# Performance work log

Measured on AMD Instinct MI355X. Metric: run time of the kernel, lower is better.

Reference implementation:

```python
import jax, jax.numpy as jnp
import numpy as np

N, E = 20000, 320000          # nodes, edges
R, B = 9, 9                   # num_relations, num_bases
IN, HID, OUT = 128, 256, 64   # feature dims
EPS = 1e-5                    # LayerNorm eps


def layer_norm(h, gamma, beta):
    mu = jnp.mean(h, axis=-1, keepdims=True)
    var = jnp.var(h, axis=-1, keepdims=True)
    return (h - mu) * jax.lax.rsqrt(var + EPS) * gamma + beta


def rgcn_conv(x, src, dst, etype, bases, comp, root, bias, aggr):
    # basis decomposition: W_r = sum_b comp[r,b] * bases[b]
    W = jnp.einsum('rb,bio->rio', comp, bases)          # [R, in, out]
    xW = jnp.einsum('ni,rio->rno', x, W)                # [R, N, out]
    msg = xW[etype, src]                                # [E, out] gather per edge
    if aggr == 'max':
        agg = jax.ops.segment_max(msg, dst, num_segments=N)
        agg = jnp.where(jnp.isfinite(agg), agg, 0.0)    # empty segments -> 0
    else:
        agg = jax.ops.segment_sum(msg, dst, num_segments=N)
    return agg + x @ root + bias


def setup_inputs() -> dict:
    key = jax.random.key(0)
    ks = jax.random.split(key, 12)
    rn = lambda k, s, sc=0.05: jax.random.normal(k, s, jnp.float32) * sc
    return {
        'x': jax.random.normal(ks[0], (N, IN), jnp.float32),
        'edge_index': jax.random.randint(ks[1], (2, E), 0, N),
        'edge_type': jax.random.randint(ks[2], (E,), 0, R),
        # conv1 params
        'bases1': rn(ks[3], (B, IN, HID)),
        'comp1': rn(ks[4], (R, B), 0.3),
        'root1': rn(ks[5], (IN, HID)),
        'bias1': jnp.zeros((HID,), jnp.float32),
        'g1': jnp.ones((HID,), jnp.float32),
        'b1': jnp.zeros((HID,), jnp.float32),
        # conv2 params
        'bases2': rn(ks[6], (B, HID, OUT)),
        'comp2': rn(ks[7], (R, B), 0.3),
        'root2': rn(ks[8], (HID, OUT)),
        'bias2': jnp.zeros((OUT,), jnp.float32),
        'g2': jnp.ones((OUT,), jnp.float32),
        'b2': jnp.zeros((OUT,), jnp.float32),
    }


def reference(x, edge_index, edge_type, bases1, comp1, root1, bias1, g1, b1,
              bases2, comp2, root2, bias2, g2, b2):
    src, dst = edge_index[0], edge_index[1]
    h = rgcn_conv(x, src, dst, edge_type, bases1, comp1, root1, bias1, 'max')
    h = jax.nn.relu(layer_norm(h, g1, b1))
    # eval mode: edge dropout and feature dropout are identity
    h = rgcn_conv(h, src, dst, edge_type, bases2, comp2, root2, bias2, 'add')
    h = layer_norm(h, g2, b2)
    return jax.nn.log_softmax(h, axis=1)
```

## Files before the change

kernel.cpp:

```cpp
#include <hip/hip_runtime.h>
#include <math.h>

#define NN 20000
#define NE 320000
#define NREL 9
#define NBASES 9
#define D_IN 128
#define D_HID 256
#define D_OUT 64
#define LN_EPS 1e-5f

#define N1 (NREL * D_HID + D_HID)
#define N2 (NREL * D_OUT + D_OUT)
#define NBLK ((NN + 255) / 256)

typedef __attribute__((ext_vector_type(8))) short bf16x8;
typedef __attribute__((ext_vector_type(4))) float f32x4;

__device__ inline ushort f2b(float f) {
    unsigned u = __float_as_uint(f);
    return (ushort)((u + 0x7FFFu + ((u >> 16) & 1u)) >> 16);
}
__device__ inline float b2f(ushort h) { return __uint_as_float(((unsigned)h) << 16); }
__device__ inline unsigned pack2bf(float f0, float f1) {
    return (unsigned)f2b(f0) | ((unsigned)f2b(f1) << 16);
}

__global__ __launch_bounds__(256) void prep_all(
    const float* __restrict__ bases1, const float* __restrict__ comp1, const float* __restrict__ root1,
    const float* __restrict__ bases2, const float* __restrict__ comp2, const float* __restrict__ root2,
    const float* __restrict__ x,
    ushort* __restrict__ w1t, ushort* __restrict__ w2t, ushort* __restrict__ xbf)
{
    const int SZ1 = N1 * D_IN;
    const int SZ2 = N2 * D_HID;
    const int SZX = NN * D_IN;
    int tid = blockIdx.x * 256 + threadIdx.x;
    if (tid < SZ1) {
        int n = tid >> 7, k = tid & 127;
        float s;
        if (n < NREL * D_HID) {
            int r = n >> 8, o = n & 255;
            s = 0.f;
            #pragma unroll
            for (int b = 0; b < NBASES; b++)
                s += comp1[r * NBASES + b] * bases1[(b * D_IN + k) * D_HID + o];
        } else {
            s = root1[k * D_HID + (n - NREL * D_HID)];
        }
        w1t[tid] = f2b(s);
    } else if (tid < SZ1 + SZ2) {
        int j = tid - SZ1;
        int n = j >> 8, k = j & 255;
        float s;
        if (n < NREL * D_OUT) {
            int r = n >> 6, o = n & 63;
            s = 0.f;
            #pragma unroll
            for (int b = 0; b < NBASES; b++)
                s += comp2[r * NBASES + b] * bases2[(b * D_HID + k) * D_OUT + o];
        } else {
            s = root2[k * D_OUT + (n - NREL * D_OUT)];
        }
        w2t[j] = f2b(s);
    } else if (tid < SZ1 + SZ2 + SZX) {
        int j = tid - SZ1 - SZ2;
        xbf[j] = f2b(x[j]);
    }
}

__global__ __launch_bounds__(256) void hist_dst(const int* __restrict__ dst, int* __restrict__ deg)
{
    int e = blockIdx.x * 256 + threadIdx.x;
    if (e < NE) atomicAdd(&deg[dst[e]], 1);
}

__global__ __launch_bounds__(256) void scan_blk(
    const int* __restrict__ deg, int* __restrict__ local, int* __restrict__ bsum)
{
    __shared__ int wsum[4];
    int tid = threadIdx.x, lane = tid & 63, w = tid >> 6;
    int i = blockIdx.x * 256 + tid;
    int v = (i < NN) ? deg[i] : 0;
    int x = v;
    #pragma unroll
    for (int d = 1; d < 64; d <<= 1) {
        int y = __shfl_up(x, d, 64);
        if (lane >= d) x += y;
    }
    if (lane == 63) wsum[w] = x;
    __syncthreads();
    int woff = 0;
    for (int j = 0; j < w; j++) woff += wsum[j];
    if (i < NN) local[i] = woff + x - v;
    if (tid == 255) bsum[blockIdx.x] = woff + x;
}

__global__ __launch_bounds__(64) void scan_top(const int* __restrict__ bsum, int* __restrict__ boff)
{
    int lane = threadIdx.x;
    int carry = 0;
    for (int base = 0; base < NBLK; base += 64) {
        int i = base + lane;
        int v = (i < NBLK) ? bsum[i] : 0;
        int x = v;
        #pragma unroll
        for (int d = 1; d < 64; d <<= 1) {
            int y = __shfl_up(x, d, 64);
            if (lane >= d) x += y;
        }
        if (i < NBLK) boff[i] = carry + x - v;
        carry += __shfl(x, 63, 64);
    }
}

__global__ __launch_bounds__(256) void scan_fin(
    const int* __restrict__ local, const int* __restrict__ boff,
    int* __restrict__ offs, int* __restrict__ cursor)
{
    int i = blockIdx.x * 256 + threadIdx.x;
    if (i < NN) {
        int o = local[i] + boff[i >> 8];
        offs[i] = o;
        cursor[i] = o;
    }
    if (i == NN) offs[NN] = NE;
}

__global__ __launch_bounds__(256) void scatter_ep(
    const int* __restrict__ src, const int* __restrict__ dst, const int* __restrict__ etype,
    int* __restrict__ cursor, int* __restrict__ ep1, int* __restrict__ ep2)
{
    int e = blockIdx.x * 256 + threadIdx.x;
    if (e >= NE) return;
    int d = dst[e];
    int s = src[e], r = etype[e];
    int pos = atomicAdd(&cursor[d], 1);
    ep1[pos] = s * N1 + r * D_HID;
    ep2[pos] = s * N2 + r * D_OUT;
}

__global__ __launch_bounds__(256) void gemm_bf16(
    const ushort* __restrict__ A, const ushort* __restrict__ Bt, ushort* __restrict__ C,
    int M, int N, int K)
{
    __shared__ ushort As[512 * 8];
    __shared__ ushort Bs[512 * 8];

    int tid = threadIdx.x;
    int lane = tid & 63, w = tid >> 6;
    int wm = w >> 1, wn = w & 1;
    int row0 = blockIdx.y * 128, col0 = blockIdx.x * 128;

    int mr = lane & 15, kc = lane >> 4;
    const ushort* ga[2];
    const ushort* gb[2];
    #pragma unroll
    for (int j = 0; j < 2; j++) {
        int g = w * 2 + j;
        int row = min(row0 + g * 16 + mr, M - 1);
        ga[j] = &A[(size_t)row * K + kc * 8];
        int col = col0 + g * 16 + mr;
        gb[j] = &Bt[(size_t)col * K + kc * 8];
    }

    f32x4 acc[4][4];
    #pragma unroll
    for (int mt = 0; mt < 4; mt++)
        #pragma unroll
        for (int nt = 0; nt < 4; nt++)
            acc[mt][nt] = (f32x4){0.f, 0.f, 0.f, 0.f};

    for (int k0 = 0; k0 < K; k0 += 32) {
        #pragma unroll
        for (int j = 0; j < 2; j++) {
            int sbase = (w * 2 + j) * 64;
            __builtin_amdgcn_global_load_lds(
                (const __attribute__((address_space(1))) unsigned int*)ga[j],
                (__attribute__((address_space(3))) unsigned int*)&As[(size_t)sbase * 8],
                16, 0, 0);
            __builtin_amdgcn_global_load_lds(
                (const __attribute__((address_space(1))) unsigned int*)gb[j],
                (__attribute__((address_space(3))) unsigned int*)&Bs[(size_t)sbase * 8],
                16, 0, 0);
            ga[j] += 32;
            gb[j] += 32;
        }
        __syncthreads();

        bf16x8 af[4], bfr[4];
        #pragma unroll
        for (int mt = 0; mt < 4; mt++)
            af[mt] = *(const bf16x8*)&As[(size_t)(((wm * 4 + mt) * 64) + lane) * 8];
        #pragma unroll
        for (int nt = 0; nt < 4; nt++)
            bfr[nt] = *(const bf16x8*)&Bs[(size_t)(((wn * 4 + nt) * 64) + lane) * 8];
        #pragma unroll
        for (int mt = 0; mt < 4; mt++)
            #pragma unroll
            for (int nt = 0; nt < 4; nt++)
                acc[mt][nt] = __builtin_amdgcn_mfma_f32_16x16x32_bf16(
                    bfr[nt], af[mt], acc[mt][nt], 0, 0, 0);
        __syncthreads();
    }

    int q = lane >> 4, cm = lane & 15;
    #pragma unroll
    for (int mt = 0; mt < 4; mt++) {
        int gr = row0 + wm * 64 + mt * 16 + cm;
        if (gr < M) {
            #pragma unroll
            for (int nt = 0; nt < 4; nt++) {
                int gc = col0 + wn * 64 + nt * 16 + q * 4;
                uint2 o;
                o.x = pack2bf(acc[mt][nt][0], acc[mt][nt][1]);
                o.y = pack2bf(acc[mt][nt][2], acc[mt][nt][3]);
                *(uint2*)&C[(size_t)gr * N + gc] = o;
            }
        }
    }
}

__global__ __launch_bounds__(256) void gather1(
    const ushort* __restrict__ xw1, const int* __restrict__ offs, const int* __restrict__ ep1,
    const float* __restrict__ bias, const float* __restrict__ g, const float* __restrict__ b,
    ushort* __restrict__ h)
{
    int n = blockIdx.x * 4 + (threadIdx.x >> 6);
    if (n >= NN) return;
    int lane = threadIdx.x & 63;
    int lane4 = lane * 4;
    int e0 = __builtin_amdgcn_readfirstlane(offs[n]);
    int e1 = __builtin_amdgcn_readfirstlane(offs[n + 1]);

    float m0 = -INFINITY, m1 = -INFINITY, m2 = -INFINITY, m3 = -INFINITY;
    int e = e0;
    for (; e + 8 <= e1; e += 8) {
        int p[8];
        #pragma unroll
        for (int j = 0; j < 8; j++) p[j] = ep1[e + j];
        ushort4 v[8];
        #pragma unroll
        for (int j = 0; j < 8; j++) v[j] = *(const ushort4*)&xw1[(size_t)(p[j] + lane4)];
        #pragma unroll
        for (int j = 0; j < 8; j++) {
            m0 = fmaxf(m0, b2f(v[j].x)); m1 = fmaxf(m1, b2f(v[j].y));
            m2 = fmaxf(m2, b2f(v[j].z)); m3 = fmaxf(m3, b2f(v[j].w));
        }
    }
    for (; e + 2 <= e1; e += 2) {
        int pa = ep1[e], pb = ep1[e + 1];
        ushort4 va = *(const ushort4*)&xw1[(size_t)(pa + lane4)];
        ushort4 vb = *(const ushort4*)&xw1[(size_t)(pb + lane4)];
        m0 = fmaxf(m0, fmaxf(b2f(va.x), b2f(vb.x)));
        m1 = fmaxf(m1, fmaxf(b2f(va.y), b2f(vb.y)));
        m2 = fmaxf(m2, fmaxf(b2f(va.z), b2f(vb.z)));
        m3 = fmaxf(m3, fmaxf(b2f(va.w), b2f(vb.w)));
    }
    for (; e < e1; e++) {
        int p = ep1[e];
        ushort4 v = *(const ushort4*)&xw1[(size_t)(p + lane4)];
        m0 = fmaxf(m0, b2f(v.x)); m1 = fmaxf(m1, b2f(v.y));
        m2 = fmaxf(m2, b2f(v.z)); m3 = fmaxf(m3, b2f(v.w));
    }
    if (e1 == e0) { m0 = m1 = m2 = m3 = 0.f; }

    ushort4 rt = *(const ushort4*)&xw1[(size_t)n * N1 + NREL * D_HID + lane4];
    int c = lane4;
    float t0 = m0 + b2f(rt.x) + bias[c + 0];
    float t1 = m1 + b2f(rt.y) + bias[c + 1];
    float t2 = m2 + b2f(rt.z) + bias[c + 2];
    float t3 = m3 + b2f(rt.w) + bias[c + 3];

    float s = t0 + t1 + t2 + t3;
    float s2 = t0 * t0 + t1 * t1 + t2 * t2 + t3 * t3;
    #pragma unroll
    for (int m = 32; m >= 1; m >>= 1) {
        s  += __shfl_xor(s,  m, 64);
        s2 += __shfl_xor(s2, m, 64);
    }
    float mu = s * (1.f / D_HID);
    float var = s2 * (1.f / D_HID) - mu * mu;
    float rs = rsqrtf(var + LN_EPS);

    ushort4 o;
    o.x = f2b(fmaxf((t0 - mu) * rs * g[c + 0] + b[c + 0], 0.f));
    o.y = f2b(fmaxf((t1 - mu) * rs * g[c + 1] + b[c + 1], 0.f));
    o.z = f2b(fmaxf((t2 - mu) * rs * g[c + 2] + b[c + 2], 0.f));
    o.w = f2b(fmaxf((t3 - mu) * rs * g[c + 3] + b[c + 3], 0.f));
    *(ushort4*)&h[(size_t)n * D_HID + c] = o;
}

__global__ __launch_bounds__(256) void gather2(
    const ushort* __restrict__ xw2, const int* __restrict__ offs, const int* __restrict__ ep2,
    const float* __restrict__ bias, const float* __restrict__ g, const float* __restrict__ b,
    float* __restrict__ out)
{
    int n = blockIdx.x * 4 + (threadIdx.x >> 6);
    if (n >= NN) return;
    int lane = threadIdx.x & 63;
    int e0 = __builtin_amdgcn_readfirstlane(offs[n]);
    int e1 = __builtin_amdgcn_readfirstlane(offs[n + 1]);

    float s = 0.f;
    int e = e0;
    for (; e + 4 <= e1; e += 4) {
        int p0 = ep2[e + 0], p1 = ep2[e + 1], p2 = ep2[e + 2], p3 = ep2[e + 3];
        float a0 = b2f(xw2[(size_t)(p0 + lane)]);
        float a1 = b2f(xw2[(size_t)(p1 + lane)]);
        float a2 = b2f(xw2[(size_t)(p2 + lane)]);
        float a3 = b2f(xw2[(size_t)(p3 + lane)]);
        s += (a0 + a1) + (a2 + a3);
    }
    for (; e < e1; e++) {
        s += b2f(xw2[(size_t)(ep2[e] + lane)]);
    }
    float v = s + b2f(xw2[(size_t)n * N2 + NREL * D_OUT + lane]) + bias[lane];

    float sm = v, s2 = v * v;
    #pragma unroll
    for (int m = 32; m >= 1; m >>= 1) {
        sm += __shfl_xor(sm, m, 64);
        s2 += __shfl_xor(s2, m, 64);
    }
    float mu = sm * (1.f / D_OUT);
    float var = s2 * (1.f / D_OUT) - mu * mu;
    float y = (v - mu) * rsqrtf(var + LN_EPS) * g[lane] + b[lane];

    float mx = y;
    #pragma unroll
    for (int m = 32; m >= 1; m >>= 1) mx = fmaxf(mx, __shfl_xor(mx, m, 64));
    float ex = __expf(y - mx);
    float se = ex;
    #pragma unroll
    for (int m = 32; m >= 1; m >>= 1) se += __shfl_xor(se, m, 64);
    out[(size_t)n * D_OUT + lane] = y - mx - logf(se);
}

extern "C" void kernel_launch(void* const* d_in, const int* in_sizes, int n_in,
                              void* d_out, int out_size, void* d_ws, size_t ws_size,
                              hipStream_t stream)
{
    const float* x      = (const float*)d_in[0];
    const int*   eidx   = (const int*)  d_in[1];
    const int*   etype  = (const int*)  d_in[2];
    const float* bases1 = (const float*)d_in[3];
    const float* comp1  = (const float*)d_in[4];
    const float* root1  = (const float*)d_in[5];
    const float* bias1  = (const float*)d_in[6];
    const float* g1     = (const float*)d_in[7];
    const float* b1     = (const float*)d_in[8];
    const float* bases2 = (const float*)d_in[9];
    const float* comp2  = (const float*)d_in[10];
    const float* root2  = (const float*)d_in[11];
    const float* bias2  = (const float*)d_in[12];
    const float* g2     = (const float*)d_in[13];
    const float* b2     = (const float*)d_in[14];

    const int* src = eidx;
    const int* dst = eidx + NE;

    char* p = (char*)d_ws;
    auto alloc = [&](size_t bytes) -> char* {
        char* r = p;
        p += (bytes + 255) & ~(size_t)255;
        return r;
    };
    ushort* xbf    = (ushort*)alloc((size_t)NN * D_IN * 2);
    ushort* w1t    = (ushort*)alloc((size_t)N1 * D_IN * 2);
    ushort* w2t    = (ushort*)alloc((size_t)N2 * D_HID * 2);
    ushort* xw1    = (ushort*)alloc((size_t)NN * N1 * 2);
    ushort* xw2    = (ushort*)alloc((size_t)NN * N2 * 2);
    ushort* h      = (ushort*)alloc((size_t)NN * D_HID * 2);
    int*    deg    = (int*)   alloc((size_t)NN * 4);
    int*    local  = (int*)   alloc((size_t)NN * 4);
    int*    bsum   = (int*)   alloc((size_t)NBLK * 4);
    int*    boff   = (int*)   alloc((size_t)NBLK * 4);
    int*    offs   = (int*)   alloc((size_t)(NN + 1) * 4);
    int*    cursor = (int*)   alloc((size_t)NN * 4);
    int*    ep1    = (int*)   alloc((size_t)NE * 4);
    int*    ep2    = (int*)   alloc((size_t)NE * 4);

    const int SZP = N1 * D_IN + N2 * D_HID + NN * D_IN;
    prep_all<<<(SZP + 255) / 256, 256, 0, stream>>>(
        bases1, comp1, root1, bases2, comp2, root2, x, w1t, w2t, xbf);

    hipMemsetAsync(deg, 0, (size_t)NN * 4, stream);
    hist_dst<<<(NE + 255) / 256, 256, 0, stream>>>(dst, deg);
    scan_blk<<<NBLK, 256, 0, stream>>>(deg, local, bsum);
    scan_top<<<1, 64, 0, stream>>>(bsum, boff);
    scan_fin<<<NBLK, 256, 0, stream>>>(local, boff, offs, cursor);
    scatter_ep<<<(NE + 255) / 256, 256, 0, stream>>>(src, dst, etype, cursor, ep1, ep2);

    gemm_bf16<<<dim3(N1 / 128, (NN + 127) / 128), 256, 0, stream>>>(xbf, w1t, xw1, NN, N1, D_IN);
    gather1<<<(NN + 3) / 4, 256, 0, stream>>>(xw1, offs, ep1, bias1, g1, b1, h);

    gemm_bf16<<<dim3(N2 / 128, (NN + 127) / 128), 256, 0, stream>>>(h, w2t, xw2, NN, N2, D_HID);
    gather2<<<(NN + 3) / 4, 256, 0, stream>>>(xw2, offs, ep2, bias2, g2, b2, (float*)d_out);
}
```

Baseline: 273.9 us.

## Double-buffer GEMM LDS tiles with register prefetch and padded row stride

```diff
diff --git a/kernel.cpp b/kernel.cpp
--- a/kernel.cpp
+++ b/kernel.cpp
@@ -13,6 +13,8 @@
 #define N1 (NREL * D_HID + D_HID)
 #define N2 (NREL * D_OUT + D_OUT)
 #define NBLK ((NN + 255) / 256)
+
+#define LSTR 40
 
 typedef __attribute__((ext_vector_type(8))) short bf16x8;
 typedef __attribute__((ext_vector_type(4))) float f32x4;
@@ -144,25 +146,23 @@
     const ushort* __restrict__ A, const ushort* __restrict__ Bt, ushort* __restrict__ C,
     int M, int N, int K)
 {
-    __shared__ ushort As[512 * 8];
-    __shared__ ushort Bs[512 * 8];
+    __shared__ ushort As[2][128 * LSTR];
+    __shared__ ushort Bs[2][128 * LSTR];
 
     int tid = threadIdx.x;
     int lane = tid & 63, w = tid >> 6;
     int wm = w >> 1, wn = w & 1;
     int row0 = blockIdx.y * 128, col0 = blockIdx.x * 128;
 
-    int mr = lane & 15, kc = lane >> 4;
-    const ushort* ga[2];
-    const ushort* gb[2];
-    #pragma unroll
-    for (int j = 0; j < 2; j++) {
-        int g = w * 2 + j;
-        int row = min(row0 + g * 16 + mr, M - 1);
-        ga[j] = &A[(size_t)row * K + kc * 8];
-        int col = col0 + g * 16 + mr;
-        gb[j] = &Bt[(size_t)col * K + kc * 8];
-    }
+    int r0 = tid >> 2, q0 = tid & 3;
+    int arow0 = min(row0 + r0, M - 1);
+    int arow1 = min(row0 + r0 + 64, M - 1);
+    const ushort* gA0 = &A[(size_t)arow0 * K + q0 * 8];
+    const ushort* gA1 = &A[(size_t)arow1 * K + q0 * 8];
+    const ushort* gB0 = &Bt[(size_t)(col0 + r0) * K + q0 * 8];
+    const ushort* gB1 = &Bt[(size_t)(col0 + r0 + 64) * K + q0 * 8];
+    int lo0 = r0 * LSTR + q0 * 8;
+    int lo1 = (r0 + 64) * LSTR + q0 * 8;
 
     f32x4 acc[4][4];
     #pragma unroll
@@ -171,37 +171,52 @@
         for (int nt = 0; nt < 4; nt++)
             acc[mt][nt] = (f32x4){0.f, 0.f, 0.f, 0.f};
 
-    for (int k0 = 0; k0 < K; k0 += 32) {
-        #pragma unroll
-        for (int j = 0; j < 2; j++) {
-            int sbase = (w * 2 + j) * 64;
-            __builtin_amdgcn_global_load_lds(
-                (const __attribute__((address_space(1))) unsigned int*)ga[j],
-                (__attribute__((address_space(3))) unsigned int*)&As[(size_t)sbase * 8],
-                16, 0, 0);
-            __builtin_amdgcn_global_load_lds(
-                (const __attribute__((address_space(1))) unsigned int*)gb[j],
-                (__attribute__((address_space(3))) unsigned int*)&Bs[(size_t)sbase * 8],
-                16, 0, 0);
-            ga[j] += 32;
-            gb[j] += 32;
-        }
+    {
+        bf16x8 a0 = *(const bf16x8*)gA0;
+        bf16x8 a1 = *(const bf16x8*)gA1;
+        bf16x8 b0 = *(const bf16x8*)gB0;
+        bf16x8 b1 = *(const bf16x8*)gB1;
+        *(bf16x8*)&As[0][lo0] = a0;
+        *(bf16x8*)&As[0][lo1] = a1;
+        *(bf16x8*)&Bs[0][lo0] = b0;
+        *(bf16x8*)&Bs[0][lo1] = b1;
+    }
+
+    int mr = lane & 15, kq = lane >> 4;
+    const int NC = K >> 5;
+    for (int c = 0; c < NC; c++) {
         __syncthreads();
+        int cur = c & 1, nxt = cur ^ 1;
+        bf16x8 a0, a1, b0, b1;
+        bool more = (c + 1 < NC);
+        if (more) {
+            gA0 += 32; gA1 += 32; gB0 += 32; gB1 += 32;
+            a0 = *(const bf16x8*)gA0;
+            a1 = *(const bf16x8*)gA1;
+            b0 = *(const bf16x8*)gB0;
+            b1 = *(const bf16x8*)gB1;
+        }
 
         bf16x8 af[4], bfr[4];
         #pragma unroll
         for (int mt = 0; mt < 4; mt++)
-            af[mt] = *(const bf16x8*)&As[(size_t)(((wm * 4 + mt) * 64) + lane) * 8];
+            af[mt] = *(const bf16x8*)&As[cur][(wm * 64 + mt * 16 + mr) * LSTR + kq * 8];
         #pragma unroll
         for (int nt = 0; nt < 4; nt++)
-            bfr[nt] = *(const bf16x8*)&Bs[(size_t)(((wn * 4 + nt) * 64) + lane) * 8];
+            bfr[nt] = *(const bf16x8*)&Bs[cur][(wn * 64 + nt * 16 + mr) * LSTR + kq * 8];
         #pragma unroll
         for (int mt = 0; mt < 4; mt++)
             #pragma unroll
             for (int nt = 0; nt < 4; nt++)
                 acc[mt][nt] = __builtin_amdgcn_mfma_f32_16x16x32_bf16(
                     bfr[nt], af[mt], acc[mt][nt], 0, 0, 0);
-        __syncthreads();
+
+        if (more) {
+            *(bf16x8*)&As[nxt][lo0] = a0;
+            *(bf16x8*)&As[nxt][lo1] = a1;
+            *(bf16x8*)&Bs[nxt][lo0] = b0;
+            *(bf16x8*)&Bs[nxt][lo1] = b1;
+        }
     }
 
     int q = lane >> 4, cm = lane & 15;
```

Measured after the change: 256.6 us. -6.3%, faster.
